# Performance work log

Measured on AMD Instinct MI355X. Metric: run time of the kernel, lower is better.

Reference implementation:

```python
import jax, jax.numpy as jnp
import numpy as np
from math import sqrt

B, L, D, NH = 1, 2048, 1024, 16
HD = D // NH
EPS = 1e-5
NEG = -1e9


def setup_inputs() -> dict:
    key = jax.random.key(0)
    ks = jax.random.split(key, 5)
    x = jax.random.normal(ks[0], (B, L, D), jnp.float32)
    # causal additive mask (added to raw QK^T scores before /sqrt(d))
    causal = jnp.tril(jnp.ones((L, L), bool))
    m = jnp.where(causal, 0.0, NEG).astype(jnp.float32)[None, None]  # (1,1,L,L)
    init = lambda k, s: (0.02 * jax.random.normal(k, s)).astype(jnp.float32)
    return dict(
        x=x, m=m,
        wx_w=init(ks[1], (3 * D, D)), wx_b=jnp.zeros((3 * D,), jnp.float32),
        wo_w=init(ks[2], (D, D)), wo_b=jnp.zeros((D,), jnp.float32),
        ffn1_w=init(ks[3], (4 * D, D)), ffn1_b=jnp.zeros((4 * D,), jnp.float32),
        ffn2_w=init(ks[4], (D, 4 * D)), ffn2_b=jnp.zeros((D,), jnp.float32),
        ln1_w=jnp.float32(1.0), ln1_b=jnp.float32(0.0),
        ln2_w=jnp.float32(1.0), ln2_b=jnp.float32(0.0),
    )


def layer_norm(x, w, b):
    # scalar gain/bias, biased variance via E[x^2] - E[x]^2 (as in source)
    mu = x.mean(-1, keepdims=True)
    mu2 = (x * x).mean(-1, keepdims=True)
    sigma = jnp.sqrt(mu2 - mu * mu + EPS)
    return w * (x - mu) / sigma + b


def gelu(x):
    return x * 0.5 * (1 + jax.scipy.special.erf(x / sqrt(2.0)))


def reference(x, m, wx_w, wx_b, wo_w, wo_b, ffn1_w, ffn1_b, ffn2_w, ffn2_b,
              ln1_w, ln1_b, ln2_w, ln2_b):
    b, l, d = x.shape
    qkv = layer_norm(x, ln1_w, ln1_b) @ wx_w.T + wx_b          # (b,l,3d)
    q, k, v = [t.reshape(b, l, NH, HD) for t in jnp.split(qkv, 3, axis=-1)]
    # mask added BEFORE scaling by 1/sqrt(d) -- faithful to source
    scores = (jnp.einsum('bind,bjnd->bnij', q, k) + m) / sqrt(d)  # (b,nh,l,l)
    A = jax.nn.softmax(scores, axis=-1)
    mha = jnp.einsum('bnij,bjnd->bind', A, v).reshape(b, l, d)
    x = x + mha @ wo_w.T + wo_b
    h = layer_norm(x, ln2_w, ln2_b)
    return x + gelu(h @ ffn1_w.T + ffn1_b) @ ffn2_w.T + ffn2_b
```

## Files before the change

### kernel.cpp

```cpp
#include <hip/hip_runtime.h>

typedef short bf16x8 __attribute__((ext_vector_type(8)));
typedef float f32x4 __attribute__((ext_vector_type(4)));
typedef unsigned short u16;

__device__ __forceinline__ u16 f2b(float f) {
  unsigned u = __builtin_bit_cast(unsigned, f);
  u += 0x7fffu + ((u >> 16) & 1u);
  return (u16)(u >> 16);
}
__device__ __forceinline__ float b2f(u16 h) {
  unsigned u = ((unsigned)h) << 16;
  return __builtin_bit_cast(float, u);
}

__device__ __forceinline__ void gload16(const void* g, void* l) {
  __builtin_amdgcn_global_load_lds(
      (const __attribute__((address_space(1))) unsigned*)g,
      (__attribute__((address_space(3))) unsigned*)l, 16, 0, 0);
}

__global__ __launch_bounds__(256) void cvt4(
    const float* __restrict__ s0, int n0, const float* __restrict__ s1, int n1,
    const float* __restrict__ s2, int n2, const float* __restrict__ s3, int n3,
    u16* __restrict__ d0, u16* __restrict__ d1, u16* __restrict__ d2, u16* __restrict__ d3) {
  long long total = ((long long)n0 + n1 + n2 + n3) >> 2;
  long long stride = (long long)gridDim.x * 256;
  for (long long i = (long long)blockIdx.x * 256 + threadIdx.x; i < total; i += stride) {
    long long e = i << 2;
    const float* s; u16* d; long long off;
    if (e < n0)                { s = s0; d = d0; off = e; }
    else if (e < n0 + n1)      { s = s1; d = d1; off = e - n0; }
    else if (e < n0 + n1 + n2) { s = s2; d = d2; off = e - n0 - n1; }
    else                       { s = s3; d = d3; off = e - n0 - n1 - n2; }
    float4 v = *(const float4*)(s + off);
    ushort4 o;
    o.x = f2b(v.x); o.y = f2b(v.y); o.z = f2b(v.z); o.w = f2b(v.w);
    *(ushort4*)(d + off) = o;
  }
}

__global__ __launch_bounds__(256) void ln_kernel(
    const float* __restrict__ x, u16* __restrict__ out,
    const float* __restrict__ wp, const float* __restrict__ bp) {
  int row = blockIdx.x;
  const float* xr = x + (size_t)row * 1024;
  float4 v = ((const float4*)xr)[threadIdx.x];
  float s = v.x + v.y + v.z + v.w;
  float s2 = v.x * v.x + v.y * v.y + v.z * v.z + v.w * v.w;
#pragma unroll
  for (int off = 32; off; off >>= 1) {
    s += __shfl_down(s, off);
    s2 += __shfl_down(s2, off);
  }
  __shared__ float red[8];
  int wv_ = threadIdx.x >> 6, ln_ = threadIdx.x & 63;
  if (ln_ == 0) { red[wv_] = s; red[4 + wv_] = s2; }
  __syncthreads();
  if (threadIdx.x == 0) {
    float ts = red[0] + red[1] + red[2] + red[3];
    float ts2 = red[4] + red[5] + red[6] + red[7];
    red[0] = ts; red[4] = ts2;
  }
  __syncthreads();
  float mu = red[0] * (1.0f / 1024.0f);
  float mu2 = red[4] * (1.0f / 1024.0f);
  float inv = 1.0f / sqrtf(mu2 - mu * mu + 1e-5f);
  float gw = *wp, gb = *bp;
  ushort4 o;
  o.x = f2b(gw * (v.x - mu) * inv + gb);
  o.y = f2b(gw * (v.y - mu) * inv + gb);
  o.z = f2b(gw * (v.z - mu) * inv + gb);
  o.w = f2b(gw * (v.w - mu) * inv + gb);
  ((ushort4*)out)[(size_t)row * 256 + threadIdx.x] = o;
}

__global__ __launch_bounds__(256) void reduce2(
    const float* __restrict__ p, const float* __restrict__ bias,
    const float* __restrict__ resid, float* __restrict__ out) {
  int i = blockIdx.x * 256 + threadIdx.x;
  float4 a = ((const float4*)p)[i];
  float4 b = ((const float4*)p)[i + 524288];
  float4 r = ((const float4*)resid)[i];
  float4 bb = ((const float4*)bias)[i & 255];
  float4 o;
  o.x = a.x + b.x + r.x + bb.x;
  o.y = a.y + b.y + r.y + bb.y;
  o.z = a.z + b.z + r.z + bb.z;
  o.w = a.w + b.w + r.w + bb.w;
  ((float4*)out)[i] = o;
}

__global__ __launch_bounds__(256) void reduce_ln(
    const float* __restrict__ p, const float* __restrict__ bias,
    const float* __restrict__ resid, float* __restrict__ x1out,
    u16* __restrict__ lnout,
    const float* __restrict__ wp, const float* __restrict__ bp) {
  int row = blockIdx.x;
  int i = row * 256 + threadIdx.x;
  float4 a = ((const float4*)p)[i];
  float4 b = ((const float4*)p)[i + 524288];
  float4 r = ((const float4*)resid)[i];
  float4 bb = ((const float4*)bias)[threadIdx.x];
  float4 v;
  v.x = a.x + b.x + r.x + bb.x;
  v.y = a.y + b.y + r.y + bb.y;
  v.z = a.z + b.z + r.z + bb.z;
  v.w = a.w + b.w + r.w + bb.w;
  ((float4*)x1out)[i] = v;
  float s = v.x + v.y + v.z + v.w;
  float s2 = v.x * v.x + v.y * v.y + v.z * v.z + v.w * v.w;
#pragma unroll
  for (int off = 32; off; off >>= 1) {
    s += __shfl_down(s, off);
    s2 += __shfl_down(s2, off);
  }
  __shared__ float red[8];
  int wv_ = threadIdx.x >> 6, ln_ = threadIdx.x & 63;
  if (ln_ == 0) { red[wv_] = s; red[4 + wv_] = s2; }
  __syncthreads();
  if (threadIdx.x == 0) {
    float ts = red[0] + red[1] + red[2] + red[3];
    float ts2 = red[4] + red[5] + red[6] + red[7];
    red[0] = ts; red[4] = ts2;
  }
  __syncthreads();
  float mu = red[0] * (1.0f / 1024.0f);
  float mu2 = red[4] * (1.0f / 1024.0f);
  float inv = 1.0f / sqrtf(mu2 - mu * mu + 1e-5f);
  float gw = *wp, gb = *bp;
  ushort4 o;
  o.x = f2b(gw * (v.x - mu) * inv + gb);
  o.y = f2b(gw * (v.y - mu) * inv + gb);
  o.z = f2b(gw * (v.z - mu) * inv + gb);
  o.w = f2b(gw * (v.w - mu) * inv + gb);
  ((ushort4*)lnout)[i] = o;
}

#define BN 128
#define BMT 64
#define BK 64

template <int EPI, bool SPLITX>
__global__ __launch_bounds__(256, 3) void gemm_bt(
    const u16* __restrict__ A, const u16* __restrict__ W,
    const float* __restrict__ bias, const float* __restrict__ resid,
    void* __restrict__ Cout, u16* __restrict__ vtout, int M, int N, int K) {
  constexpr int MR = BMT / 32;
  __shared__ __align__(16) u16 sA[2][BMT * BK];
  __shared__ __align__(16) u16 sB[2][BN * BK];
  const int tid = threadIdx.x;

  const int gx = gridDim.x, gy = gridDim.y;
  int bx, by;
  {
    int oxy = blockIdx.y * gx + blockIdx.x;
    int xcd = oxy & 7, pos = oxy >> 3;
    if (SPLITX) {
      int bxp = gx >> 3;
      bx = xcd * bxp + pos % bxp;
      by = pos / bxp;
    } else {
      int byp = gy >> 3;
      by = xcd * byp + pos % byp;
      bx = pos / byp;
    }
  }

  const int l = tid & 63;
  const int w = tid >> 6;
  const int wm = w >> 1, wn = w & 1;
  const int lr = l & 15, lg = l >> 4;

  f32x4 acc[MR][4] = {};

  const int r_st = tid >> 3;
  const int s_st = tid & 7;

  const u16* Abase = A + (size_t)(by * BMT) * K;
  const u16* Wbase = W + (size_t)(bx * BN) * K;
  const int NK = K / (BK * (int)gridDim.z);
  const int ktbase = (int)blockIdx.z * NK;

  auto stage = [&](int buf, int kt) {
    const int k0 = (ktbase + kt) * BK;
#pragma unroll
    for (int i = 0; i < BMT / 32; i++) {
      int r = i * 32 + r_st;
      int ss = s_st ^ (r & 7);
      gload16(Abase + (size_t)r * K + k0 + ss * 8, &sA[buf][(i * 256 + tid) * 8]);
    }
#pragma unroll
    for (int i = 0; i < 4; i++) {
      int r = i * 32 + r_st;
      int ss = s_st ^ (r & 7);
      gload16(Wbase + (size_t)r * K + k0 + ss * 8, &sB[buf][(i * 256 + tid) * 8]);
    }
  };

  auto compute = [&](int buf) {
#pragma unroll
    for (int kk = 0; kk < 2; kk++) {
      bf16x8 a[MR], b[4];
#pragma unroll
      for (int mr = 0; mr < MR; mr++) {
        int row = wm * (BMT / 2) + mr * 16 + lr;
        int ss = (kk * 4 + lg) ^ (row & 7);
        a[mr] = *(const bf16x8*)&sA[buf][row * 64 + ss * 8];
      }
#pragma unroll
      for (int nr = 0; nr < 4; nr++) {
        int row = wn * 64 + nr * 16 + lr;
        int ss = (kk * 4 + lg) ^ (row & 7);
        b[nr] = *(const bf16x8*)&sB[buf][row * 64 + ss * 8];
      }
#pragma unroll
      for (int mr = 0; mr < MR; mr++)
#pragma unroll
        for (int nr = 0; nr < 4; nr++)
          acc[mr][nr] = __builtin_amdgcn_mfma_f32_16x16x32_bf16(a[mr], b[nr], acc[mr][nr], 0, 0, 0);
    }
  };

  stage(0, 0);
  asm volatile("s_waitcnt vmcnt(0)" ::: "memory");
  __syncthreads();
  for (int kt = 0; kt < NK; kt++) {
    if (kt + 1 < NK) stage((kt + 1) & 1, kt + 1);
    compute(kt & 1);
    asm volatile("s_waitcnt vmcnt(0)" ::: "memory");
    __syncthreads();
  }

  const int crow0 = by * BMT + wm * (BMT / 2);
  const int ccol0 = bx * BN + wn * 64;

  if (EPI == 4) {
    float* P4 = (float*)Cout + (size_t)blockIdx.z * (size_t)M * N;
#pragma unroll
    for (int nr = 0; nr < 4; nr++) {
      int col = ccol0 + nr * 16 + lr;
#pragma unroll
      for (int mr = 0; mr < MR; mr++) {
        int rowb = crow0 + mr * 16 + lg * 4;
#pragma unroll
        for (int r = 0; r < 4; r++)
          P4[(size_t)(rowb + r) * N + col] = acc[mr][nr][r];
      }
    }
    return;
  }

  if (EPI == 3 && ccol0 >= 2048) {
    const int hd0 = ccol0 - 2048;
#pragma unroll
    for (int nr = 0; nr < 4; nr++) {
      int hd = hd0 + nr * 16 + lr;
      float bv = bias[ccol0 + nr * 16 + lr];
#pragma unroll
      for (int mr = 0; mr < MR; mr++) {
        int m0 = crow0 + mr * 16 + lg * 4;
        ushort4 o;
        o.x = f2b(acc[mr][nr][0] + bv);
        o.y = f2b(acc[mr][nr][1] + bv);
        o.z = f2b(acc[mr][nr][2] + bv);
        o.w = f2b(acc[mr][nr][3] + bv);
        *(ushort4*)&vtout[(size_t)hd * 2048 + m0] = o;
      }
    }
    return;
  }

#pragma unroll
  for (int nr = 0; nr < 4; nr++) {
    int col = ccol0 + nr * 16 + lr;
    float bv = bias[col];
#pragma unroll
    for (int mr = 0; mr < MR; mr++) {
      int rowb = crow0 + mr * 16 + lg * 4;
#pragma unroll
      for (int r = 0; r < 4; r++) {
        float v = acc[mr][nr][r] + bv;
        size_t off = (size_t)(rowb + r) * N + col;
        if (EPI == 2) {
          float g = 0.5f * v * (1.0f + erff(v * 0.70710678118f));
          ((u16*)Cout)[off] = f2b(g);
        } else {
          ((u16*)Cout)[off] = f2b(v);
        }
      }
    }
  }
}

__global__ __launch_bounds__(256) void attn_kernel(
    const u16* __restrict__ qkv, const u16* __restrict__ vt,
    u16* __restrict__ mha) {
  const int qb = (int)gridDim.x - 1 - (int)blockIdx.x;
  const int h = blockIdx.y;
  __shared__ __align__(16) u16 sK[2][64 * 64];
  __shared__ __align__(16) u16 sV[2][64 * 64];
  __shared__ __align__(16) u16 P[4][16 * 72];
  const int tid = threadIdx.x;
  const int l = tid & 63, w = tid >> 6;
  const int lr = l & 15, lg = l >> 4;
  const int qrow0 = qb * 64 + w * 16;
  const u16* kbase = qkv + 1024 + h * 64;
  const u16* vbase = vt + (size_t)(h * 64) * 2048;

  const int r_st = tid >> 3;
  const int s_st = tid & 7;

  auto stage = [&](int buf, int t) {
    const int j0 = t * 64;
#pragma unroll
    for (int i = 0; i < 2; i++) {
      int r = i * 32 + r_st;
      int ss = s_st ^ (r & 7);
      gload16(kbase + (size_t)(j0 + r) * 3072 + ss * 8, &sK[buf][(i * 256 + tid) * 8]);
    }
#pragma unroll
    for (int i = 0; i < 2; i++) {
      int r = i * 32 + r_st;
      int ss = s_st ^ (r & 7);
      gload16(vbase + (size_t)r * 2048 + j0 + ss * 8, &sV[buf][(i * 256 + tid) * 8]);
    }
  };

  bf16x8 aq[2];
#pragma unroll
  for (int kk = 0; kk < 2; kk++)
    aq[kk] = *(const bf16x8*)&qkv[(size_t)(qrow0 + lr) * 3072 + h * 64 + kk * 32 + lg * 8];

  f32x4 oa[4];
  float l_r[4] = {0.f, 0.f, 0.f, 0.f};
#pragma unroll
  for (int d = 0; d < 4; d++) oa[d] = f32x4{0.f, 0.f, 0.f, 0.f};

  auto compute = [&](int buf, int t, bool masked) {
    const int j0 = t * 64;
    f32x4 s[4] = {};
#pragma unroll
    for (int kk = 0; kk < 2; kk++) {
#pragma unroll
      for (int c = 0; c < 4; c++) {
        int row = c * 16 + lr;
        int ss = (kk * 4 + lg) ^ (row & 7);
        bf16x8 kf = *(const bf16x8*)&sK[buf][row * 64 + ss * 8];
        s[c] = __builtin_amdgcn_mfma_f32_16x16x32_bf16(aq[kk], kf, s[c], 0, 0, 0);
      }
    }

#pragma unroll
    for (int r = 0; r < 4; r++) {
      const int q = qrow0 + lg * 4 + r;
      float rs = 0.f;
#pragma unroll
      for (int c = 0; c < 4; c++) {
        float p = __expf(s[c][r] * 0.03125f);
        if (masked) {
          int j = j0 + c * 16 + lr;
          p = (j > q) ? 0.f : p;
        }
        u16 pb = f2b(p);
        P[w][(lg * 4 + r) * 72 + c * 16 + lr] = pb;
        rs += b2f(pb);
      }
      l_r[r] += rs;
    }

#pragma unroll
    for (int kk = 0; kk < 2; kk++) {
      bf16x8 pa = *(const bf16x8*)&P[w][lr * 72 + kk * 32 + lg * 8];
#pragma unroll
      for (int d = 0; d < 4; d++) {
        int row = d * 16 + lr;
        int ss = (kk * 4 + lg) ^ (row & 7);
        bf16x8 bv = *(const bf16x8*)&sV[buf][row * 64 + ss * 8];
        oa[d] = __builtin_amdgcn_mfma_f32_16x16x32_bf16(pa, bv, oa[d], 0, 0, 0);
      }
    }
  };

  const int nt = qb + 1;
  stage(0, 0);
  asm volatile("s_waitcnt vmcnt(0)" ::: "memory");
  __syncthreads();
  for (int t = 0; t < nt; t++) {
    if (t + 1 < nt) stage((t + 1) & 1, t + 1);
    compute(t & 1, t, t == nt - 1);
    asm volatile("s_waitcnt vmcnt(0)" ::: "memory");
    __syncthreads();
  }

#pragma unroll
  for (int r = 0; r < 4; r++) {
#pragma unroll
    for (int off = 1; off < 16; off <<= 1) l_r[r] += __shfl_xor(l_r[r], off);
    float inv = 1.0f / l_r[r];
    int q = qrow0 + lg * 4 + r;
#pragma unroll
    for (int d = 0; d < 4; d++)
      mha[(size_t)q * 1024 + h * 64 + d * 16 + lr] = f2b(oa[d][r] * inv);
  }
}

extern "C" void kernel_launch(void* const* d_in, const int* in_sizes, int n_in,
                              void* d_out, int out_size, void* d_ws, size_t ws_size,
                              hipStream_t stream) {
  const float* x    = (const float*)d_in[0];
  const float* wx_w = (const float*)d_in[2];
  const float* wx_b = (const float*)d_in[3];
  const float* wo_w = (const float*)d_in[4];
  const float* wo_b = (const float*)d_in[5];
  const float* f1_w = (const float*)d_in[6];
  const float* f1_b = (const float*)d_in[7];
  const float* f2_w = (const float*)d_in[8];
  const float* f2_b = (const float*)d_in[9];
  const float* ln1w = (const float*)d_in[10];
  const float* ln1b = (const float*)d_in[11];
  const float* ln2w = (const float*)d_in[12];
  const float* ln2b = (const float*)d_in[13];

  char* ws = (char*)d_ws;
  u16*   ln_x  = (u16*)(ws + 0);
  u16*   qkv   = (u16*)(ws + 4194304);
  float* part  = (float*)(ws + 0);
  u16*   mhab  = (u16*)(ws + 16777216);
  float* x1    = (float*)(ws + 20971520);
  u16*   hbuf  = (u16*)(ws + 29360128);
  u16*   vt    = (u16*)(ws + 33554432);
  u16*   f1o   = (u16*)(ws + 33554432);
  u16*   wxb16 = (u16*)(ws + 50331648);
  u16*   wob16 = (u16*)(ws + 56623104);
  u16*   f1b16 = (u16*)(ws + 58720256);
  u16*   f2b16 = (u16*)(ws + 67108864);

  cvt4<<<1024, 256, 0, stream>>>(wx_w, 3145728, wo_w, 1048576, f1_w, 4194304, f2_w, 4194304,
                                 wxb16, wob16, f1b16, f2b16);
  ln_kernel<<<2048, 256, 0, stream>>>(x, ln_x, ln1w, ln1b);
  gemm_bt<3, true><<<dim3(24, 32), 256, 0, stream>>>(ln_x, wxb16, wx_b, nullptr, qkv, vt, 2048, 3072, 1024);
  attn_kernel<<<dim3(32, 16), 256, 0, stream>>>(qkv, vt, mhab);
  gemm_bt<4, false><<<dim3(8, 32, 2), 256, 0, stream>>>(mhab, wob16, wo_b, nullptr, part, nullptr, 2048, 1024, 1024);
  reduce_ln<<<2048, 256, 0, stream>>>(part, wo_b, x, x1, hbuf, ln2w, ln2b);
  gemm_bt<2, true><<<dim3(32, 32), 256, 0, stream>>>(hbuf, f1b16, f1_b, nullptr, f1o, nullptr, 2048, 4096, 1024);
  gemm_bt<4, false><<<dim3(8, 32, 2), 256, 0, stream>>>(f1o, f2b16, f2_b, nullptr, part, nullptr, 2048, 1024, 4096);
  reduce2<<<2048, 256, 0, stream>>>(part, f2_b, x1, (float*)d_out);
}
```

Before: 168.0 us.

## Split long causal attention rows across two blocks and combine partial sums

```diff
diff --git a/kernel.cpp b/kernel.cpp
--- a/kernel.cpp
+++ b/kernel.cpp
@@ -295,8 +295,17 @@
 
 __global__ __launch_bounds__(256) void attn_kernel(
     const u16* __restrict__ qkv, const u16* __restrict__ vt,
-    u16* __restrict__ mha) {
-  const int qb = (int)gridDim.x - 1 - (int)blockIdx.x;
+    float* __restrict__ O0, float* __restrict__ O1,
+    float* __restrict__ l0p, float* __restrict__ l1p) {
+  const int i = (int)blockIdx.x;
+  int qb, sidx;
+  if (i < 32) { qb = 31 - (i >> 1); sidx = i & 1; }
+  else        { qb = 47 - i;        sidx = 0;     }
+  const int nt = qb + 1;
+  const int h0 = (i < 32) ? ((nt + 1) >> 1) : nt;
+  const int t0 = sidx ? h0 : 0;
+  const int t1 = sidx ? nt : h0;
+
   const int h = blockIdx.y;
   __shared__ __align__(16) u16 sK[2][64 * 64];
   __shared__ __align__(16) u16 sV[2][64 * 64];
@@ -314,16 +323,16 @@
   auto stage = [&](int buf, int t) {
     const int j0 = t * 64;
 #pragma unroll
-    for (int i = 0; i < 2; i++) {
-      int r = i * 32 + r_st;
+    for (int i2 = 0; i2 < 2; i2++) {
+      int r = i2 * 32 + r_st;
       int ss = s_st ^ (r & 7);
-      gload16(kbase + (size_t)(j0 + r) * 3072 + ss * 8, &sK[buf][(i * 256 + tid) * 8]);
-    }
-#pragma unroll
-    for (int i = 0; i < 2; i++) {
-      int r = i * 32 + r_st;
+      gload16(kbase + (size_t)(j0 + r) * 3072 + ss * 8, &sK[buf][(i2 * 256 + tid) * 8]);
+    }
+#pragma unroll
+    for (int i2 = 0; i2 < 2; i2++) {
+      int r = i2 * 32 + r_st;
       int ss = s_st ^ (r & 7);
-      gload16(vbase + (size_t)r * 2048 + j0 + ss * 8, &sV[buf][(i * 256 + tid) * 8]);
+      gload16(vbase + (size_t)r * 2048 + j0 + ss * 8, &sV[buf][(i2 * 256 + tid) * 8]);
     }
   };
 
@@ -382,27 +391,51 @@
     }
   };
 
-  const int nt = qb + 1;
-  stage(0, 0);
+  const int ntile = t1 - t0;
+  stage(0, t0);
   asm volatile("s_waitcnt vmcnt(0)" ::: "memory");
   __syncthreads();
-  for (int t = 0; t < nt; t++) {
-    if (t + 1 < nt) stage((t + 1) & 1, t + 1);
-    compute(t & 1, t, t == nt - 1);
+  for (int ti = 0; ti < ntile; ti++) {
+    const int t = t0 + ti;
+    if (ti + 1 < ntile) stage((ti + 1) & 1, t + 1);
+    compute(ti & 1, t, t == nt - 1);
     asm volatile("s_waitcnt vmcnt(0)" ::: "memory");
     __syncthreads();
   }
 
+  float* Op = sidx ? (O1 - (size_t)1024 * 1024) : O0;
+  float* lp = sidx ? (l1p - 1024 * 16) : l0p;
 #pragma unroll
   for (int r = 0; r < 4; r++) {
 #pragma unroll
     for (int off = 1; off < 16; off <<= 1) l_r[r] += __shfl_xor(l_r[r], off);
-    float inv = 1.0f / l_r[r];
     int q = qrow0 + lg * 4 + r;
+    if (lr == 0) lp[q * 16 + h] = l_r[r];
 #pragma unroll
     for (int d = 0; d < 4; d++)
-      mha[(size_t)q * 1024 + h * 64 + d * 16 + lr] = f2b(oa[d][r] * inv);
-  }
+      Op[(size_t)q * 1024 + h * 64 + d * 16 + lr] = oa[d][r];
+  }
+}
+
+__global__ __launch_bounds__(256) void attn_combine(
+    const float* __restrict__ O0, const float* __restrict__ O1,
+    const float* __restrict__ l0p, const float* __restrict__ l1p,
+    u16* __restrict__ mhab) {
+  const int row = blockIdx.x;
+  const int t = threadIdx.x;
+  const int h = t >> 4;
+  float4 v = ((const float4*)(O0 + (size_t)row * 1024))[t];
+  float ls = l0p[row * 16 + h];
+  if (row >= 1024) {
+    float4 v1 = ((const float4*)(O1 + (size_t)(row - 1024) * 1024))[t];
+    v.x += v1.x; v.y += v1.y; v.z += v1.z; v.w += v1.w;
+    ls += l1p[(row - 1024) * 16 + h];
+  }
+  float inv = 1.0f / ls;
+  ushort4 o;
+  o.x = f2b(v.x * inv); o.y = f2b(v.y * inv);
+  o.z = f2b(v.z * inv); o.w = f2b(v.w * inv);
+  ((ushort4*)(mhab + (size_t)row * 1024))[t] = o;
 }
 
 extern "C" void kernel_launch(void* const* d_in, const int* in_sizes, int n_in,
@@ -424,11 +457,15 @@
 
   char* ws = (char*)d_ws;
   u16*   ln_x  = (u16*)(ws + 0);
+  float* l0p   = (float*)(ws + 0);
+  float* l1p   = (float*)(ws + 131072);
   u16*   qkv   = (u16*)(ws + 4194304);
   float* part  = (float*)(ws + 0);
   u16*   mhab  = (u16*)(ws + 16777216);
   float* x1    = (float*)(ws + 20971520);
+  float* O0    = (float*)(ws + 20971520);
   u16*   hbuf  = (u16*)(ws + 29360128);
+  float* O1    = (float*)(ws + 29360128);
   u16*   vt    = (u16*)(ws + 33554432);
   u16*   f1o   = (u16*)(ws + 33554432);
   u16*   wxb16 = (u16*)(ws + 50331648);
@@ -440,7 +477,8 @@
                                  wxb16, wob16, f1b16, f2b16);
   ln_kernel<<<2048, 256, 0, stream>>>(x, ln_x, ln1w, ln1b);
   gemm_bt<3, true><<<dim3(24, 32), 256, 0, stream>>>(ln_x, wxb16, wx_b, nullptr, qkv, vt, 2048, 3072, 1024);
-  attn_kernel<<<dim3(32, 16), 256, 0, stream>>>(qkv, vt, mhab);
+  attn_kernel<<<dim3(48, 16), 256, 0, stream>>>(qkv, vt, O0, O1, l0p, l1p);
+  attn_combine<<<2048, 256, 0, stream>>>(O0, O1, l0p, l1p, mhab);
   gemm_bt<4, false><<<dim3(8, 32, 2), 256, 0, stream>>>(mhab, wob16, wo_b, nullptr, part, nullptr, 2048, 1024, 1024);
   reduce_ln<<<2048, 256, 0, stream>>>(part, wo_b, x, x1, hbuf, ln2w, ln2b);
   gemm_bt<2, true><<<dim3(32, 32), 256, 0, stream>>>(hbuf, f1b16, f1_b, nullptr, f1o, nullptr, 2048, 4096, 1024);
```

Result: faster. 161.7 us (-3.8%).
